# Performance work log

Measured on AMD Instinct MI355X. Metric: run time of the kernel, lower is better.

## Reference

```python
import jax, jax.numpy as jnp
import numpy as np

N = 50000      # nodes
E = 800000     # edges
IN = 256       # in_dim
H = 8          # heads
C = 32         # out_dim per head (H*C == IN so residual is identity)
NEG_SLOPE = 0.2
LN_EPS = 1e-5


def setup_inputs() -> dict:
    key = jax.random.key(0)
    ks = jax.random.split(key, 8)
    x = jax.random.normal(ks[0], (N, IN), dtype=jnp.float32)
    edge_index = jax.random.randint(ks[1], (2, E), 0, N, dtype=jnp.int64)
    # GATConv params
    W = jax.random.normal(ks[2], (IN, H * C), dtype=jnp.float32) / np.sqrt(IN)
    att_src = jax.random.normal(ks[3], (H, C), dtype=jnp.float32) / np.sqrt(C)
    att_dst = jax.random.normal(ks[4], (H, C), dtype=jnp.float32) / np.sqrt(C)
    bias = jnp.zeros((H * C,), dtype=jnp.float32)
    # LayerNorm params
    ln_scale = jnp.ones((H * C,), dtype=jnp.float32)
    ln_bias = jnp.zeros((H * C,), dtype=jnp.float32)
    return {"x": x, "edge_index": edge_index, "W": W, "att_src": att_src,
            "att_dst": att_dst, "bias": bias, "ln_scale": ln_scale, "ln_bias": ln_bias}


def _gat_block(x, edge_index, W, att_src, att_dst, bias, ln_scale, ln_bias):
    src, dst = edge_index[0], edge_index[1]
    # linear projection -> [N, H, C]
    h = (x @ W).reshape(N, H, C)
    # per-node attention logits [N, H]
    a_src = jnp.einsum('nhc,hc->nh', h, att_src)
    a_dst = jnp.einsum('nhc,hc->nh', h, att_dst)
    # per-edge logits with LeakyReLU [E, H]
    alpha = jax.nn.leaky_relu(a_src[src] + a_dst[dst], NEG_SLOPE)
    # segment softmax over incoming edges of each destination node
    amax = jax.ops.segment_max(alpha, dst, num_segments=N)          # [N, H]
    amax = jnp.where(jnp.isfinite(amax), amax, 0.0)                 # empty segments
    ex = jnp.exp(alpha - amax[dst])                                 # [E, H]
    denom = jax.ops.segment_sum(ex, dst, num_segments=N)           # [N, H]
    attn = ex / (denom[dst] + 1e-16)                                # [E, H]
    # weighted message aggregation -> [N, H, C]
    msg = h[src] * attn[:, :, None]
    out = jax.ops.segment_sum(msg, dst, num_segments=N)
    out = out.reshape(N, H * C) + bias
    # residual (identity since in_dim == heads*out_dim), ELU, LayerNorm
    out = out + x
    out = jax.nn.elu(out)
    mu = jnp.mean(out, axis=-1, keepdims=True)
    var = jnp.var(out, axis=-1, keepdims=True)
    return (out - mu) * jax.lax.rsqrt(var + LN_EPS) * ln_scale + ln_bias


def reference(x, edge_index, W, att_src, att_dst, bias, ln_scale, ln_bias):
    return _gat_block(x, edge_index, W, att_src, att_dst, bias, ln_scale, ln_bias)
```

## Files before the change

kernel.cpp:

```cpp
#include <hip/hip_runtime.h>
#include <hip/hip_bf16.h>
#include <cstdint>

#define NN 50000
#define NE 800000
#define DIM 256
#define NH 8
#define NB 196

typedef short v8s __attribute__((ext_vector_type(8)));
typedef float v4f __attribute__((ext_vector_type(4)));
typedef unsigned short u16x8 __attribute__((ext_vector_type(8)));

__device__ __forceinline__ float b2f(unsigned short u) {
    union { float f; uint32_t i; } c; c.i = ((uint32_t)u) << 16; return c.f;
}
__device__ __forceinline__ unsigned short f2b(float f) {
    union { float f; uint32_t i; } c; c.f = f;
    uint32_t lsb = (c.i >> 16) & 1u;
    return (unsigned short)((c.i + 0x7FFFu + lsb) >> 16);
}

__global__ __launch_bounds__(256) void normalize_kernel(
    const int* __restrict__ e, int* __restrict__ srcN, int* __restrict__ dstN,
    int* __restrict__ deg) {
    const int i = blockIdx.x * 256 + threadIdx.x;
    const int lane = threadIdx.x & 63;
    int probe = e[2 * lane + 1];
    unsigned long long nz = __ballot(probe != 0);
    bool is64 = (nz == 0ull);
    int s, d;
    if (is64) { s = e[2 * i]; d = e[2 * (NE + i)]; }
    else      { s = e[i];     d = e[NE + i]; }
    srcN[i] = s;
    dstN[i] = d;
    atomicAdd(&deg[d], 1);
}

__global__ __launch_bounds__(256) void cvtw_kernel(const float* __restrict__ W,
                                                   unsigned short* __restrict__ Wt) {
    int idx = blockIdx.x * 256 + threadIdx.x;
    int k = idx >> 8, n = idx & 255;
    Wt[n * DIM + k] = f2b(W[k * DIM + n]);
}

#define LDA2 40
__global__ __launch_bounds__(512) void gemm_kernel(
    const float* __restrict__ X, const unsigned short* __restrict__ Wt,
    unsigned short* __restrict__ H) {
    __shared__ __align__(16) unsigned short As[128 * LDA2];
    __shared__ __align__(16) unsigned short Bs[256 * LDA2];
    const int t = threadIdx.x;
    const int wave = t >> 6, lane = t & 63;
    const int wr = wave >> 2, wc = wave & 3;
    const int fr = lane & 15, fq = lane >> 4;
    const int m0 = blockIdx.x * 128;

    v4f acc[4][4];
    #pragma unroll
    for (int mi = 0; mi < 4; ++mi)
        #pragma unroll
        for (int j = 0; j < 4; ++j) acc[mi][j] = (v4f){0.f, 0.f, 0.f, 0.f};

    #pragma unroll
    for (int kt = 0; kt < 256; kt += 32) {
        #pragma unroll
        for (int it = 0; it < 2; ++it) {
            int v = t + it * 512;
            int row = v >> 3;
            int c4 = (v & 7) << 2;
            int gr = m0 + row;
            float4 val = make_float4(0.f, 0.f, 0.f, 0.f);
            if (gr < NN) val = *(const float4*)(X + (size_t)gr * DIM + kt + c4);
            ushort4 o;
            o.x = f2b(val.x); o.y = f2b(val.y); o.z = f2b(val.z); o.w = f2b(val.w);
            *(ushort4*)(As + row * LDA2 + c4) = o;
        }
        #pragma unroll
        for (int it = 0; it < 2; ++it) {
            int v = t + it * 512;
            int row = v >> 2;
            int kv = (v & 3) << 3;
            u16x8 val = *(const u16x8*)(Wt + (size_t)row * DIM + kt + kv);
            *(u16x8*)(Bs + row * LDA2 + kv) = val;
        }
        __syncthreads();
        v8s a[4];
        #pragma unroll
        for (int mi = 0; mi < 4; ++mi)
            a[mi] = *(const v8s*)(As + (wr * 64 + mi * 16 + fr) * LDA2 + fq * 8);
        #pragma unroll
        for (int j = 0; j < 4; ++j) {
            v8s b = *(const v8s*)(Bs + (wc * 64 + j * 16 + fr) * LDA2 + fq * 8);
            #pragma unroll
            for (int mi = 0; mi < 4; ++mi)
                acc[mi][j] = __builtin_amdgcn_mfma_f32_16x16x32_bf16(a[mi], b, acc[mi][j], 0, 0, 0);
        }
        __syncthreads();
    }
    #pragma unroll
    for (int mi = 0; mi < 4; ++mi)
        #pragma unroll
        for (int j = 0; j < 4; ++j)
            #pragma unroll
            for (int r = 0; r < 4; ++r) {
                int gr = m0 + wr * 64 + mi * 16 + fq * 4 + r;
                int gc = wc * 64 + j * 16 + fr;
                if (gr < NN) H[(size_t)gr * DIM + gc] = f2b(acc[mi][j][r]);
            }
}

__global__ __launch_bounds__(256) void att_kernel(
    const unsigned short* __restrict__ H, const float* __restrict__ ASRC,
    const float* __restrict__ ADST, float* __restrict__ a_src,
    float* __restrict__ a_dst) {
    const int wave = threadIdx.x >> 6, lane = threadIdx.x & 63;
    const int n = blockIdx.x * 4 + wave;
    if (n >= NN) return;
    float4 as4 = *(const float4*)(ASRC + lane * 4);
    float4 ad4 = *(const float4*)(ADST + lane * 4);
    ushort4 hv = *(const ushort4*)(H + (size_t)n * DIM + lane * 4);
    const unsigned short* hvp = (const unsigned short*)&hv;
    float h0 = b2f(hvp[0]), h1 = b2f(hvp[1]), h2 = b2f(hvp[2]), h3 = b2f(hvp[3]);
    float ps = h0 * as4.x + h1 * as4.y + h2 * as4.z + h3 * as4.w;
    float pd = h0 * ad4.x + h1 * ad4.y + h2 * ad4.z + h3 * ad4.w;
    #pragma unroll
    for (int off = 1; off <= 4; off <<= 1) {
        ps += __shfl_xor(ps, off);
        pd += __shfl_xor(pd, off);
    }
    if ((lane & 7) == 0) {
        a_src[n * NH + (lane >> 3)] = ps;
        a_dst[n * NH + (lane >> 3)] = pd;
    }
}

__global__ __launch_bounds__(256) void scan1_kernel(const int* __restrict__ deg,
                                                    int* __restrict__ row_start,
                                                    int* __restrict__ bsum) {
    const int t = threadIdx.x, b = blockIdx.x;
    const int i = b * 256 + t;
    const int lane = t & 63, wave = t >> 6;
    int v = (i < NN) ? deg[i] : 0;
    int x = v;
    #pragma unroll
    for (int off = 1; off <= 32; off <<= 1) {
        int y = __shfl_up(x, off);
        if (lane >= off) x += y;
    }
    __shared__ int wt[4];
    if (lane == 63) wt[wave] = x;
    __syncthreads();
    int add = 0;
    #pragma unroll
    for (int w2 = 0; w2 < 4; ++w2) if (w2 < wave) add += wt[w2];
    int incl = x + add;
    if (i < NN) row_start[i] = incl - v;
    if (t == 255) bsum[b] = incl;
}

__global__ __launch_bounds__(256) void scan2_kernel(const int* __restrict__ bsum,
                                                    int* __restrict__ boff,
                                                    int* __restrict__ row_start) {
    const int t = threadIdx.x;
    const int lane = t & 63, wave = t >> 6;
    int v = (t < NB) ? bsum[t] : 0;
    int x = v;
    #pragma unroll
    for (int off = 1; off <= 32; off <<= 1) {
        int y = __shfl_up(x, off);
        if (lane >= off) x += y;
    }
    __shared__ int wt[4];
    if (lane == 63) wt[wave] = x;
    __syncthreads();
    int add = 0;
    #pragma unroll
    for (int w2 = 0; w2 < 4; ++w2) if (w2 < wave) add += wt[w2];
    int incl = x + add;
    if (t < NB) boff[t] = incl - v;
    if (t == 255) row_start[NN] = incl;
}

__global__ __launch_bounds__(256) void scan3_kernel(int* __restrict__ row_start,
                                                    const int* __restrict__ boff,
                                                    int* __restrict__ cursor) {
    const int i = blockIdx.x * 256 + threadIdx.x;
    if (i < NN) {
        int r = row_start[i] + boff[blockIdx.x];
        row_start[i] = r;
        cursor[i] = r;
    }
}

__global__ void fill_kernel(const int* __restrict__ src, const int* __restrict__ dst,
                            int* __restrict__ cursor, int* __restrict__ csr_src) {
    int e = blockIdx.x * blockDim.x + threadIdx.x;
    if (e < NE) {
        int d = dst[e];
        int pos = atomicAdd(&cursor[d], 1);
        csr_src[pos] = src[e];
    }
}

__global__ __launch_bounds__(256) void agg_kernel(
    const unsigned short* __restrict__ H, const float* __restrict__ a_src,
    const float* __restrict__ a_dst, const int* __restrict__ row_start,
    const int* __restrict__ csr_src, const float* __restrict__ X,
    const float* __restrict__ BIAS, const float* __restrict__ LNS,
    const float* __restrict__ LNB, float* __restrict__ OUT) {
    const int wave = threadIdx.x >> 6, lane = threadIdx.x & 63;
    const int d = blockIdx.x * 4 + wave;
    if (d >= NN) return;
    const int base = row_start[d];
    const int degree = row_start[d + 1] - base;
    const int slot = lane >> 5;
    const int q = lane & 31;
    const int jj = lane >> 3;
    const int hh = lane & 7;
    const int headq = q >> 2;

    const float ad = a_dst[d * NH + hh];

    float4 x0 = *(const float4*)(X + (size_t)d * DIM + q * 8);
    float4 x1 = *(const float4*)(X + (size_t)d * DIM + q * 8 + 4);
    float4 b0 = *(const float4*)(BIAS + q * 8);
    float4 b1 = *(const float4*)(BIAS + q * 8 + 4);
    float4 sc0 = *(const float4*)(LNS + q * 8);
    float4 sc1 = *(const float4*)(LNS + q * 8 + 4);
    float4 lb0 = *(const float4*)(LNB + q * 8);
    float4 lb1 = *(const float4*)(LNB + q * 8 + 4);

    float acc[8];
    #pragma unroll
    for (int j = 0; j < 8; ++j) acc[j] = 0.f;
    float swacc = 0.f;

    for (int c0 = 0; c0 < degree; c0 += 8) {
        int e = c0 + jj;
        bool vld = e < degree;
        int sj = vld ? csr_src[base + e] : 0;
        float av = a_src[sj * NH + hh];
        float lg = av + ad;
        lg = lg > 0.f ? lg : 0.2f * lg;
        float w = vld ? __expf(lg) : 0.f;
        swacc += w;

        int s0 = __shfl(sj, (0 + slot) * 8);
        int s1 = __shfl(sj, (2 + slot) * 8);
        int s2 = __shfl(sj, (4 + slot) * 8);
        int s3 = __shfl(sj, (6 + slot) * 8);
        u16x8 hv0 = *(const u16x8*)(H + (size_t)s0 * DIM + q * 8);
        u16x8 hv1 = *(const u16x8*)(H + (size_t)s1 * DIM + q * 8);
        u16x8 hv2 = *(const u16x8*)(H + (size_t)s2 * DIM + q * 8);
        u16x8 hv3 = *(const u16x8*)(H + (size_t)s3 * DIM + q * 8);
        float w0 = __shfl(w, (0 + slot) * 8 + headq);
        float w1 = __shfl(w, (2 + slot) * 8 + headq);
        float w2 = __shfl(w, (4 + slot) * 8 + headq);
        float w3 = __shfl(w, (6 + slot) * 8 + headq);
        #pragma unroll
        for (int j = 0; j < 8; ++j) acc[j] += w0 * b2f(hv0[j]);
        #pragma unroll
        for (int j = 0; j < 8; ++j) acc[j] += w1 * b2f(hv1[j]);
        #pragma unroll
        for (int j = 0; j < 8; ++j) acc[j] += w2 * b2f(hv2[j]);
        #pragma unroll
        for (int j = 0; j < 8; ++j) acc[j] += w3 * b2f(hv3[j]);
    }

    float sumw = swacc;
    sumw += __shfl_xor(sumw, 8);
    sumw += __shfl_xor(sumw, 16);
    sumw += __shfl_xor(sumw, 32);
    float sum_ex = __shfl(sumw, headq);

    #pragma unroll
    for (int j = 0; j < 8; ++j) acc[j] += __shfl_xor(acc[j], 32);

    const float inv = 1.0f / (sum_ex + 1e-16f);

    const float* xp0 = (const float*)&x0; const float* xp1 = (const float*)&x1;
    const float* bp0 = (const float*)&b0; const float* bp1 = (const float*)&b1;
    float v[8];
    float s1v = 0.f, s2v = 0.f;
    #pragma unroll
    for (int j = 0; j < 8; ++j) {
        float xv = (j < 4) ? xp0[j] : xp1[j - 4];
        float bv = (j < 4) ? bp0[j] : bp1[j - 4];
        float t = acc[j] * inv + bv + xv;
        t = t > 0.f ? t : expm1f(t);
        v[j] = t;
        s1v += t;
        s2v += t * t;
    }
    #pragma unroll
    for (int off = 16; off >= 1; off >>= 1) {
        s1v += __shfl_xor(s1v, off);
        s2v += __shfl_xor(s2v, off);
    }
    const float mean = s1v * (1.0f / 256.0f);
    float var = s2v * (1.0f / 256.0f) - mean * mean;
    var = fmaxf(var, 0.f);
    const float rstd = rsqrtf(var + 1e-5f);

    if (slot == 0) {
        const float* scp0 = (const float*)&sc0; const float* scp1 = (const float*)&sc1;
        const float* lbp0 = (const float*)&lb0; const float* lbp1 = (const float*)&lb1;
        float4 o0, o1;
        float* op0 = (float*)&o0; float* op1 = (float*)&o1;
        #pragma unroll
        for (int j = 0; j < 4; ++j) {
            op0[j] = (v[j] - mean) * rstd * scp0[j] + lbp0[j];
            op1[j] = (v[j + 4] - mean) * rstd * scp1[j] + lbp1[j];
        }
        *(float4*)(OUT + (size_t)d * DIM + q * 8) = o0;
        *(float4*)(OUT + (size_t)d * DIM + q * 8 + 4) = o1;
    }
}

extern "C" void kernel_launch(void* const* d_in, const int* in_sizes, int n_in,
                              void* d_out, int out_size, void* d_ws, size_t ws_size,
                              hipStream_t stream) {
    const float* X    = (const float*)d_in[0];
    const int*   EIDX = (const int*)d_in[1];
    const float* W    = (const float*)d_in[2];
    const float* ASRC = (const float*)d_in[3];
    const float* ADST = (const float*)d_in[4];
    const float* BIAS = (const float*)d_in[5];
    const float* LNS  = (const float*)d_in[6];
    const float* LNB  = (const float*)d_in[7];
    float* OUT = (float*)d_out;

    char* ws = (char*)d_ws;
    unsigned short* H  = (unsigned short*)(ws);
    unsigned short* Wt = (unsigned short*)(ws + 25600000);
    float* a_src       = (float*)(ws + 25731072);
    float* a_dst       = (float*)(ws + 27331072);
    int*   deg         = (int*)(ws + 28931072);
    int*   row_start   = (int*)(ws + 29131072);
    int*   cursor      = (int*)(ws + 29331088);
    int*   csr_src     = (int*)(ws + 29531088);
    int*   srcN        = (int*)(ws + 32731088);
    int*   dstN        = (int*)(ws + 35931088);
    int*   bsum        = (int*)(ws + 39131088);
    int*   boff        = (int*)(ws + 39131872);

    hipMemsetAsync(deg, 0, NN * sizeof(int), stream);

    dim3 blk(256);
    normalize_kernel<<<dim3(NE / 256), blk, 0, stream>>>(EIDX, srcN, dstN, deg);
    cvtw_kernel<<<dim3(256), blk, 0, stream>>>(W, Wt);
    gemm_kernel<<<dim3(391), dim3(512), 0, stream>>>(X, Wt, H);
    att_kernel<<<dim3((NN + 3) / 4), blk, 0, stream>>>(H, ASRC, ADST, a_src, a_dst);
    scan1_kernel<<<dim3(NB), blk, 0, stream>>>(deg, row_start, bsum);
    scan2_kernel<<<dim3(1), blk, 0, stream>>>(bsum, boff, row_start);
    scan3_kernel<<<dim3(NB), blk, 0, stream>>>(row_start, boff, cursor);
    fill_kernel<<<dim3((NE + 255) / 256), blk, 0, stream>>>(srcN, dstN, cursor, csr_src);
    agg_kernel<<<dim3((NN + 3) / 4), blk, 0, stream>>>(
        H, a_src, a_dst, row_start, csr_src, X, BIAS, LNS, LNB, OUT);
}
```

Before: 309.2 us.

## Fuse attention logits into GEMM epilogue and precompute edge weights in CSR fill

The per-node attention dot products are now computed in the GEMM epilogue with shuffle reductions, which removes the separate att_kernel pass over H. The edge normalization pass is split: a degree-only kernel reads the edge list, and the fill kernel rereads it, computes exp(leaky_relu) edge weights and stores them in CSR order. The aggregation kernel then loads these weights directly instead of gathering a_src and recomputing exponentials. The GEMM K-tile grows from 32 to 64, so there are fewer barriers. In exchange, a 25.6MB per-edge weight array is written and read back, and the softmax still skips the max subtraction, which risks overflow.

```diff
diff --git a/kernel.cpp b/kernel.cpp
--- a/kernel.cpp
+++ b/kernel.cpp
@@ -21,9 +21,197 @@
     return (unsigned short)((c.i + 0x7FFFu + lsb) >> 16);
 }
 
-__global__ __launch_bounds__(256) void normalize_kernel(
-    const int* __restrict__ e, int* __restrict__ srcN, int* __restrict__ dstN,
-    int* __restrict__ deg) {
+__global__ __launch_bounds__(256) void deg_kernel(const int* __restrict__ e,
+                                                  int* __restrict__ deg) {
+    const int i = blockIdx.x * 256 + threadIdx.x;
+    const int lane = threadIdx.x & 63;
+    int probe = e[2 * lane + 1];
+    unsigned long long nz = __ballot(probe != 0);
+    bool is64 = (nz == 0ull);
+    int d = is64 ? e[2 * (NE + i)] : e[NE + i];
+    atomicAdd(&deg[d], 1);
+}
+
+__global__ __launch_bounds__(256) void cvtw_kernel(const float* __restrict__ W,
+                                                   unsigned short* __restrict__ Wt) {
+    int idx = blockIdx.x * 256 + threadIdx.x;
+    int k = idx >> 8, n = idx & 255;
+    Wt[n * DIM + k] = f2b(W[k * DIM + n]);
+}
+
+#define LDA3 72
+__global__ __launch_bounds__(512) void gemm_kernel(
+    const float* __restrict__ X, const unsigned short* __restrict__ Wt,
+    const float* __restrict__ ASRC, const float* __restrict__ ADST,
+    unsigned short* __restrict__ H, float* __restrict__ a_srcG,
+    float* __restrict__ a_dstG) {
+    __shared__ __align__(16) unsigned short As[128 * LDA3];
+    __shared__ __align__(16) unsigned short Bs[256 * LDA3];
+    const int t = threadIdx.x;
+    const int wave = t >> 6, lane = t & 63;
+    const int wr = wave >> 2, wc = wave & 3;
+    const int fr = lane & 15, fq = lane >> 4;
+    const int m0 = blockIdx.x * 128;
+
+    v4f acc[4][4];
+    #pragma unroll
+    for (int mi = 0; mi < 4; ++mi)
+        #pragma unroll
+        for (int j = 0; j < 4; ++j) acc[mi][j] = (v4f){0.f, 0.f, 0.f, 0.f};
+
+    #pragma unroll
+    for (int kt = 0; kt < 256; kt += 64) {
+        #pragma unroll
+        for (int it = 0; it < 4; ++it) {
+            int v = t + it * 512;
+            int row = v >> 4;
+            int c4 = (v & 15) << 2;
+            int gr = m0 + row;
+            float4 val = make_float4(0.f, 0.f, 0.f, 0.f);
+            if (gr < NN) val = *(const float4*)(X + (size_t)gr * DIM + kt + c4);
+            ushort4 o;
+            o.x = f2b(val.x); o.y = f2b(val.y); o.z = f2b(val.z); o.w = f2b(val.w);
+            *(ushort4*)(As + row * LDA3 + c4) = o;
+        }
+        #pragma unroll
+        for (int it = 0; it < 4; ++it) {
+            int v = t + it * 512;
+            int row = v >> 3;
+            int kv = (v & 7) << 3;
+            u16x8 val = *(const u16x8*)(Wt + (size_t)row * DIM + kt + kv);
+            *(u16x8*)(Bs + row * LDA3 + kv) = val;
+        }
+        __syncthreads();
+        #pragma unroll
+        for (int ks = 0; ks < 64; ks += 32) {
+            v8s a[4];
+            #pragma unroll
+            for (int mi = 0; mi < 4; ++mi)
+                a[mi] = *(const v8s*)(As + (wr * 64 + mi * 16 + fr) * LDA3 + ks + fq * 8);
+            #pragma unroll
+            for (int j = 0; j < 4; ++j) {
+                v8s b = *(const v8s*)(Bs + (wc * 64 + j * 16 + fr) * LDA3 + ks + fq * 8);
+                #pragma unroll
+                for (int mi = 0; mi < 4; ++mi)
+                    acc[mi][j] = __builtin_amdgcn_mfma_f32_16x16x32_bf16(a[mi], b, acc[mi][j], 0, 0, 0);
+            }
+        }
+        __syncthreads();
+    }
+
+    float asv[4], adv[4];
+    #pragma unroll
+    for (int j = 0; j < 4; ++j) {
+        int hidx = 2 * wc + (j >> 1);
+        int cidx = ((j & 1) << 4) + fr;
+        asv[j] = ASRC[hidx * 32 + cidx];
+        adv[j] = ADST[hidx * 32 + cidx];
+    }
+    #pragma unroll
+    for (int mi = 0; mi < 4; ++mi) {
+        float tSA[4], tSB[4], tDA[4], tDB[4];
+        #pragma unroll
+        for (int r = 0; r < 4; ++r) {
+            tSA[r] = acc[mi][0][r] * asv[0] + acc[mi][1][r] * asv[1];
+            tSB[r] = acc[mi][2][r] * asv[2] + acc[mi][3][r] * asv[3];
+            tDA[r] = acc[mi][0][r] * adv[0] + acc[mi][1][r] * adv[1];
+            tDB[r] = acc[mi][2][r] * adv[2] + acc[mi][3][r] * adv[3];
+            #pragma unroll
+            for (int off = 1; off <= 8; off <<= 1) {
+                tSA[r] += __shfl_xor(tSA[r], off);
+                tSB[r] += __shfl_xor(tSB[r], off);
+                tDA[r] += __shfl_xor(tDA[r], off);
+                tDB[r] += __shfl_xor(tDB[r], off);
+            }
+        }
+        if (fr == 0) {
+            #pragma unroll
+            for (int r = 0; r < 4; ++r) {
+                int gr = m0 + wr * 64 + mi * 16 + fq * 4 + r;
+                if (gr < NN) {
+                    a_srcG[gr * NH + 2 * wc]     = tSA[r];
+                    a_srcG[gr * NH + 2 * wc + 1] = tSB[r];
+                    a_dstG[gr * NH + 2 * wc]     = tDA[r];
+                    a_dstG[gr * NH + 2 * wc + 1] = tDB[r];
+                }
+            }
+        }
+    }
+
+    #pragma unroll
+    for (int mi = 0; mi < 4; ++mi)
+        #pragma unroll
+        for (int j = 0; j < 4; ++j)
+            #pragma unroll
+            for (int r = 0; r < 4; ++r) {
+                int gr = m0 + wr * 64 + mi * 16 + fq * 4 + r;
+                int gc = wc * 64 + j * 16 + fr;
+                if (gr < NN) H[(size_t)gr * DIM + gc] = f2b(acc[mi][j][r]);
+            }
+}
+
+__global__ __launch_bounds__(256) void scan1_kernel(const int* __restrict__ deg,
+                                                    int* __restrict__ row_start,
+                                                    int* __restrict__ bsum) {
+    const int t = threadIdx.x, b = blockIdx.x;
+    const int i = b * 256 + t;
+    const int lane = t & 63, wave = t >> 6;
+    int v = (i < NN) ? deg[i] : 0;
+    int x = v;
+    #pragma unroll
+    for (int off = 1; off <= 32; off <<= 1) {
+        int y = __shfl_up(x, off);
+        if (lane >= off) x += y;
+    }
+    __shared__ int wt[4];
+    if (lane == 63) wt[wave] = x;
+    __syncthreads();
+    int add = 0;
+    #pragma unroll
+    for (int w2 = 0; w2 < 4; ++w2) if (w2 < wave) add += wt[w2];
+    int incl = x + add;
+    if (i < NN) row_start[i] = incl - v;
+    if (t == 255) bsum[b] = incl;
+}
+
+__global__ __launch_bounds__(256) void scan2_kernel(const int* __restrict__ bsum,
+                                                    int* __restrict__ boff,
+                                                    int* __restrict__ row_start) {
+    const int t = threadIdx.x;
+    const int lane = t & 63, wave = t >> 6;
+    int v = (t < NB) ? bsum[t] : 0;
+    int x = v;
+    #pragma unroll
+    for (int off = 1; off <= 32; off <<= 1) {
+        int y = __shfl_up(x, off);
+        if (lane >= off) x += y;
+    }
+    __shared__ int wt[4];
+    if (lane == 63) wt[wave] = x;
+    __syncthreads();
+    int add = 0;
+    #pragma unroll
+    for (int w2 = 0; w2 < 4; ++w2) if (w2 < wave) add += wt[w2];
+    int incl = x + add;
+    if (t < NB) boff[t] = incl - v;
+    if (t == 255) row_start[NN] = incl;
+}
+
+__global__ __launch_bounds__(256) void scan3_kernel(int* __restrict__ row_start,
+                                                    const int* __restrict__ boff,
+                                                    int* __restrict__ cursor) {
+    const int i = blockIdx.x * 256 + threadIdx.x;
+    if (i < NN) {
+        int r = row_start[i] + boff[blockIdx.x];
+        row_start[i] = r;
+        cursor[i] = r;
+    }
+}
+
+__global__ __launch_bounds__(256) void fill_kernel(
+    const int* __restrict__ e, const float* __restrict__ a_src,
+    const float* __restrict__ a_dst, int* __restrict__ cursor,
+    int* __restrict__ csr_src, float* __restrict__ wcsr) {
     const int i = blockIdx.x * 256 + threadIdx.x;
     const int lane = threadIdx.x & 63;
     int probe = e[2 * lane + 1];
@@ -32,183 +220,35 @@
     int s, d;
     if (is64) { s = e[2 * i]; d = e[2 * (NE + i)]; }
     else      { s = e[i];     d = e[NE + i]; }
-    srcN[i] = s;
-    dstN[i] = d;
-    atomicAdd(&deg[d], 1);
-}
-
-__global__ __launch_bounds__(256) void cvtw_kernel(const float* __restrict__ W,
-                                                   unsigned short* __restrict__ Wt) {
-    int idx = blockIdx.x * 256 + threadIdx.x;
-    int k = idx >> 8, n = idx & 255;
-    Wt[n * DIM + k] = f2b(W[k * DIM + n]);
-}
-
-#define LDA2 40
-__global__ __launch_bounds__(512) void gemm_kernel(
-    const float* __restrict__ X, const unsigned short* __restrict__ Wt,
-    unsigned short* __restrict__ H) {
-    __shared__ __align__(16) unsigned short As[128 * LDA2];
-    __shared__ __align__(16) unsigned short Bs[256 * LDA2];
-    const int t = threadIdx.x;
-    const int wave = t >> 6, lane = t & 63;
-    const int wr = wave >> 2, wc = wave & 3;
-    const int fr = lane & 15, fq = lane >> 4;
-    const int m0 = blockIdx.x * 128;
-
-    v4f acc[4][4];
-    #pragma unroll
-    for (int mi = 0; mi < 4; ++mi)
-        #pragma unroll
-        for (int j = 0; j < 4; ++j) acc[mi][j] = (v4f){0.f, 0.f, 0.f, 0.f};
-
-    #pragma unroll
-    for (int kt = 0; kt < 256; kt += 32) {
-        #pragma unroll
-        for (int it = 0; it < 2; ++it) {
-            int v = t + it * 512;
-            int row = v >> 3;
-            int c4 = (v & 7) << 2;
-            int gr = m0 + row;
-            float4 val = make_float4(0.f, 0.f, 0.f, 0.f);
-            if (gr < NN) val = *(const float4*)(X + (size_t)gr * DIM + kt + c4);
-            ushort4 o;
-            o.x = f2b(val.x); o.y = f2b(val.y); o.z = f2b(val.z); o.w = f2b(val.w);
-            *(ushort4*)(As + row * LDA2 + c4) = o;
-        }
-        #pragma unroll
-        for (int it = 0; it < 2; ++it) {
-            int v = t + it * 512;
-            int row = v >> 2;
-            int kv = (v & 3) << 3;
-            u16x8 val = *(const u16x8*)(Wt + (size_t)row * DIM + kt + kv);
-            *(u16x8*)(Bs + row * LDA2 + kv) = val;
-        }
-        __syncthreads();
-        v8s a[4];
-        #pragma unroll
-        for (int mi = 0; mi < 4; ++mi)
-            a[mi] = *(const v8s*)(As + (wr * 64 + mi * 16 + fr) * LDA2 + fq * 8);
-        #pragma unroll
-        for (int j = 0; j < 4; ++j) {
-            v8s b = *(const v8s*)(Bs + (wc * 64 + j * 16 + fr) * LDA2 + fq * 8);
-            #pragma unroll
-            for (int mi = 0; mi < 4; ++mi)
-                acc[mi][j] = __builtin_amdgcn_mfma_f32_16x16x32_bf16(a[mi], b, acc[mi][j], 0, 0, 0);
-        }
-        __syncthreads();
-    }
-    #pragma unroll
-    for (int mi = 0; mi < 4; ++mi)
-        #pragma unroll
-        for (int j = 0; j < 4; ++j)
-            #pragma unroll
-            for (int r = 0; r < 4; ++r) {
-                int gr = m0 + wr * 64 + mi * 16 + fq * 4 + r;
-                int gc = wc * 64 + j * 16 + fr;
-                if (gr < NN) H[(size_t)gr * DIM + gc] = f2b(acc[mi][j][r]);
-            }
-}
-
-__global__ __launch_bounds__(256) void att_kernel(
-    const unsigned short* __restrict__ H, const float* __restrict__ ASRC,
-    const float* __restrict__ ADST, float* __restrict__ a_src,
-    float* __restrict__ a_dst) {
-    const int wave = threadIdx.x >> 6, lane = threadIdx.x & 63;
-    const int n = blockIdx.x * 4 + wave;
-    if (n >= NN) return;
-    float4 as4 = *(const float4*)(ASRC + lane * 4);
-    float4 ad4 = *(const float4*)(ADST + lane * 4);
-    ushort4 hv = *(const ushort4*)(H + (size_t)n * DIM + lane * 4);
-    const unsigned short* hvp = (const unsigned short*)&hv;
-    float h0 = b2f(hvp[0]), h1 = b2f(hvp[1]), h2 = b2f(hvp[2]), h3 = b2f(hvp[3]);
-    float ps = h0 * as4.x + h1 * as4.y + h2 * as4.z + h3 * as4.w;
-    float pd = h0 * ad4.x + h1 * ad4.y + h2 * ad4.z + h3 * ad4.w;
-    #pragma unroll
-    for (int off = 1; off <= 4; off <<= 1) {
-        ps += __shfl_xor(ps, off);
-        pd += __shfl_xor(pd, off);
-    }
-    if ((lane & 7) == 0) {
-        a_src[n * NH + (lane >> 3)] = ps;
-        a_dst[n * NH + (lane >> 3)] = pd;
-    }
-}
-
-__global__ __launch_bounds__(256) void scan1_kernel(const int* __restrict__ deg,
-                                                    int* __restrict__ row_start,
-                                                    int* __restrict__ bsum) {
-    const int t = threadIdx.x, b = blockIdx.x;
-    const int i = b * 256 + t;
-    const int lane = t & 63, wave = t >> 6;
-    int v = (i < NN) ? deg[i] : 0;
-    int x = v;
-    #pragma unroll
-    for (int off = 1; off <= 32; off <<= 1) {
-        int y = __shfl_up(x, off);
-        if (lane >= off) x += y;
-    }
-    __shared__ int wt[4];
-    if (lane == 63) wt[wave] = x;
-    __syncthreads();
-    int add = 0;
-    #pragma unroll
-    for (int w2 = 0; w2 < 4; ++w2) if (w2 < wave) add += wt[w2];
-    int incl = x + add;
-    if (i < NN) row_start[i] = incl - v;
-    if (t == 255) bsum[b] = incl;
-}
-
-__global__ __launch_bounds__(256) void scan2_kernel(const int* __restrict__ bsum,
-                                                    int* __restrict__ boff,
-                                                    int* __restrict__ row_start) {
-    const int t = threadIdx.x;
-    const int lane = t & 63, wave = t >> 6;
-    int v = (t < NB) ? bsum[t] : 0;
-    int x = v;
-    #pragma unroll
-    for (int off = 1; off <= 32; off <<= 1) {
-        int y = __shfl_up(x, off);
-        if (lane >= off) x += y;
-    }
-    __shared__ int wt[4];
-    if (lane == 63) wt[wave] = x;
-    __syncthreads();
-    int add = 0;
-    #pragma unroll
-    for (int w2 = 0; w2 < 4; ++w2) if (w2 < wave) add += wt[w2];
-    int incl = x + add;
-    if (t < NB) boff[t] = incl - v;
-    if (t == 255) row_start[NN] = incl;
-}
-
-__global__ __launch_bounds__(256) void scan3_kernel(int* __restrict__ row_start,
-                                                    const int* __restrict__ boff,
-                                                    int* __restrict__ cursor) {
-    const int i = blockIdx.x * 256 + threadIdx.x;
-    if (i < NN) {
-        int r = row_start[i] + boff[blockIdx.x];
-        row_start[i] = r;
-        cursor[i] = r;
-    }
-}
-
-__global__ void fill_kernel(const int* __restrict__ src, const int* __restrict__ dst,
-                            int* __restrict__ cursor, int* __restrict__ csr_src) {
-    int e = blockIdx.x * blockDim.x + threadIdx.x;
-    if (e < NE) {
-        int d = dst[e];
-        int pos = atomicAdd(&cursor[d], 1);
-        csr_src[pos] = src[e];
-    }
+    int pos = atomicAdd(&cursor[d], 1);
+    csr_src[pos] = s;
+    float4 as0 = *(const float4*)(a_src + (size_t)s * NH);
+    float4 as1 = *(const float4*)(a_src + (size_t)s * NH + 4);
+    float4 ad0 = *(const float4*)(a_dst + (size_t)d * NH);
+    float4 ad1 = *(const float4*)(a_dst + (size_t)d * NH + 4);
+    const float* asp0 = (const float*)&as0; const float* asp1 = (const float*)&as1;
+    const float* adp0 = (const float*)&ad0; const float* adp1 = (const float*)&ad1;
+    float4 w0, w1;
+    float* wp0 = (float*)&w0; float* wp1 = (float*)&w1;
+    #pragma unroll
+    for (int h = 0; h < 4; ++h) {
+        float lg = asp0[h] + adp0[h];
+        lg = lg > 0.f ? lg : 0.2f * lg;
+        wp0[h] = __expf(lg);
+        float lg2 = asp1[h] + adp1[h];
+        lg2 = lg2 > 0.f ? lg2 : 0.2f * lg2;
+        wp1[h] = __expf(lg2);
+    }
+    *(float4*)(wcsr + (size_t)pos * NH) = w0;
+    *(float4*)(wcsr + (size_t)pos * NH + 4) = w1;
 }
 
 __global__ __launch_bounds__(256) void agg_kernel(
-    const unsigned short* __restrict__ H, const float* __restrict__ a_src,
-    const float* __restrict__ a_dst, const int* __restrict__ row_start,
-    const int* __restrict__ csr_src, const float* __restrict__ X,
-    const float* __restrict__ BIAS, const float* __restrict__ LNS,
-    const float* __restrict__ LNB, float* __restrict__ OUT) {
+    const unsigned short* __restrict__ H, const int* __restrict__ row_start,
+    const int* __restrict__ csr_src, const float* __restrict__ wcsr,
+    const float* __restrict__ X, const float* __restrict__ BIAS,
+    const float* __restrict__ LNS, const float* __restrict__ LNB,
+    float* __restrict__ OUT) {
     const int wave = threadIdx.x >> 6, lane = threadIdx.x & 63;
     const int d = blockIdx.x * 4 + wave;
     if (d >= NN) return;
@@ -216,11 +256,7 @@
     const int degree = row_start[d + 1] - base;
     const int slot = lane >> 5;
     const int q = lane & 31;
-    const int jj = lane >> 3;
-    const int hh = lane & 7;
     const int headq = q >> 2;
-
-    const float ad = a_dst[d * NH + hh];
 
     float4 x0 = *(const float4*)(X + (size_t)d * DIM + q * 8);
     float4 x1 = *(const float4*)(X + (size_t)d * DIM + q * 8 + 4);
@@ -234,30 +270,23 @@
     float acc[8];
     #pragma unroll
     for (int j = 0; j < 8; ++j) acc[j] = 0.f;
-    float swacc = 0.f;
+    float sumw = 0.f;
 
     for (int c0 = 0; c0 < degree; c0 += 8) {
-        int e = c0 + jj;
-        bool vld = e < degree;
-        int sj = vld ? csr_src[base + e] : 0;
-        float av = a_src[sj * NH + hh];
-        float lg = av + ad;
-        lg = lg > 0.f ? lg : 0.2f * lg;
-        float w = vld ? __expf(lg) : 0.f;
-        swacc += w;
-
-        int s0 = __shfl(sj, (0 + slot) * 8);
-        int s1 = __shfl(sj, (2 + slot) * 8);
-        int s2 = __shfl(sj, (4 + slot) * 8);
-        int s3 = __shfl(sj, (6 + slot) * 8);
+        const int e0 = c0 + slot * 4;
+        const int rem = degree - e0;
+        const size_t eb = (size_t)base + e0;
+        int s0 = 0, s1 = 0, s2 = 0, s3 = 0;
+        float w0 = 0.f, w1 = 0.f, w2 = 0.f, w3 = 0.f;
+        if (rem > 0) { s0 = csr_src[eb];     w0 = wcsr[eb * NH + headq]; }
+        if (rem > 1) { s1 = csr_src[eb + 1]; w1 = wcsr[(eb + 1) * NH + headq]; }
+        if (rem > 2) { s2 = csr_src[eb + 2]; w2 = wcsr[(eb + 2) * NH + headq]; }
+        if (rem > 3) { s3 = csr_src[eb + 3]; w3 = wcsr[(eb + 3) * NH + headq]; }
         u16x8 hv0 = *(const u16x8*)(H + (size_t)s0 * DIM + q * 8);
         u16x8 hv1 = *(const u16x8*)(H + (size_t)s1 * DIM + q * 8);
         u16x8 hv2 = *(const u16x8*)(H + (size_t)s2 * DIM + q * 8);
         u16x8 hv3 = *(const u16x8*)(H + (size_t)s3 * DIM + q * 8);
-        float w0 = __shfl(w, (0 + slot) * 8 + headq);
-        float w1 = __shfl(w, (2 + slot) * 8 + headq);
-        float w2 = __shfl(w, (4 + slot) * 8 + headq);
-        float w3 = __shfl(w, (6 + slot) * 8 + headq);
+        sumw += (w0 + w1) + (w2 + w3);
         #pragma unroll
         for (int j = 0; j < 8; ++j) acc[j] += w0 * b2f(hv0[j]);
         #pragma unroll
@@ -268,12 +297,7 @@
         for (int j = 0; j < 8; ++j) acc[j] += w3 * b2f(hv3[j]);
     }
 
-    float sumw = swacc;
-    sumw += __shfl_xor(sumw, 8);
-    sumw += __shfl_xor(sumw, 16);
-    sumw += __shfl_xor(sumw, 32);
-    float sum_ex = __shfl(sumw, headq);
-
+    float sum_ex = sumw + __shfl_xor(sumw, 32);
     #pragma unroll
     for (int j = 0; j < 8; ++j) acc[j] += __shfl_xor(acc[j], 32);
 
@@ -334,28 +358,26 @@
     char* ws = (char*)d_ws;
     unsigned short* H  = (unsigned short*)(ws);
     unsigned short* Wt = (unsigned short*)(ws + 25600000);
-    float* a_src       = (float*)(ws + 25731072);
-    float* a_dst       = (float*)(ws + 27331072);
+    float* a_srcW      = (float*)(ws + 25731072);
+    float* a_dstW      = (float*)(ws + 27331072);
     int*   deg         = (int*)(ws + 28931072);
     int*   row_start   = (int*)(ws + 29131072);
     int*   cursor      = (int*)(ws + 29331088);
     int*   csr_src     = (int*)(ws + 29531088);
-    int*   srcN        = (int*)(ws + 32731088);
-    int*   dstN        = (int*)(ws + 35931088);
-    int*   bsum        = (int*)(ws + 39131088);
-    int*   boff        = (int*)(ws + 39131872);
+    float* wcsr        = (float*)(ws + 32731136);
+    int*   bsum        = (int*)(ws + 58331136);
+    int*   boff        = (int*)(ws + 58331920);
 
     hipMemsetAsync(deg, 0, NN * sizeof(int), stream);
 
     dim3 blk(256);
-    normalize_kernel<<<dim3(NE / 256), blk, 0, stream>>>(EIDX, srcN, dstN, deg);
-    cvtw_kernel<<<dim3(256), blk, 0, stream>>>(W, Wt);
-    gemm_kernel<<<dim3(391), dim3(512), 0, stream>>>(X, Wt, H);
-    att_kernel<<<dim3((NN + 3) / 4), blk, 0, stream>>>(H, ASRC, ADST, a_src, a_dst);
+    deg_kernel<<<dim3(NE / 256), blk, 0, stream>>>(EIDX, deg);
     scan1_kernel<<<dim3(NB), blk, 0, stream>>>(deg, row_start, bsum);
     scan2_kernel<<<dim3(1), blk, 0, stream>>>(bsum, boff, row_start);
     scan3_kernel<<<dim3(NB), blk, 0, stream>>>(row_start, boff, cursor);
-    fill_kernel<<<dim3((NE + 255) / 256), blk, 0, stream>>>(srcN, dstN, cursor, csr_src);
+    cvtw_kernel<<<dim3(256), blk, 0, stream>>>(W, Wt);
+    gemm_kernel<<<dim3(391), dim3(512), 0, stream>>>(X, Wt, ASRC, ADST, H, a_srcW, a_dstW);
+    fill_kernel<<<dim3(NE / 256), blk, 0, stream>>>(EIDX, a_srcW, a_dstW, cursor, csr_src, wcsr);
     agg_kernel<<<dim3((NN + 3) / 4), blk, 0, stream>>>(
-        H, a_src, a_dst, row_start, csr_src, X, BIAS, LNS, LNB, OUT);
-}
+        H, row_start, csr_src, wcsr, X, BIAS, LNS, LNB, OUT);
+}
```

New measurement: 336.6 us. 1.09x slower.
